# Kernel optimization log

Measured on AMD Instinct MI355X. Metric: run time of the kernel, lower is better.

## Reference

```python
import jax, jax.numpy as jnp
import numpy as np

N_NODES = 8192


def _gcn_norm(edge_index, num_nodes):
    # PyG GCNConv default: add self-loops, symmetric normalization.
    src, dst = edge_index[0], edge_index[1]
    loop = jnp.arange(num_nodes, dtype=src.dtype)
    src = jnp.concatenate([src, loop])
    dst = jnp.concatenate([dst, loop])
    deg = jax.ops.segment_sum(jnp.ones_like(dst, dtype=jnp.float32), dst,
                              num_segments=num_nodes)
    dis = jnp.where(deg > 0, jax.lax.rsqrt(jnp.maximum(deg, 1.0)), 0.0)
    norm = dis[src] * dis[dst]  # [E + N]
    return src, dst, norm


def _gcn_conv(x, W, b, src, dst, norm, num_nodes):
    h = x @ W                           # [N, F_out] dense GEMM
    msg = h[src] * norm[:, None]        # gather + scale, [E+N, F_out]
    out = jax.ops.segment_sum(msg, dst, num_segments=num_nodes)  # scatter-add
    return out + b


def setup_inputs() -> dict:
    key = jax.random.key(0)
    ks = jax.random.split(key, 8)
    N, E, F_in, H1, H2, F_out = N_NODES, 65536, 512, 4096, 1024, 10
    x = jax.random.normal(ks[0], (N, F_in), dtype=jnp.float32)
    edge_index = jax.random.randint(ks[1], (2, E), 0, N, dtype=jnp.int64)
    # Glorot-ish scaled weights
    W1 = jax.random.normal(ks[2], (F_in, H1), dtype=jnp.float32) * (1.0 / np.sqrt(F_in))
    b1 = jnp.zeros((H1,), dtype=jnp.float32)
    W2 = jax.random.normal(ks[3], (H1, H2), dtype=jnp.float32) * (1.0 / np.sqrt(H1))
    b2 = jnp.zeros((H2,), dtype=jnp.float32)
    W3 = jax.random.normal(ks[4], (H2, F_out), dtype=jnp.float32) * (1.0 / np.sqrt(H2))
    b3 = jnp.zeros((F_out,), dtype=jnp.float32)
    return {"x": x, "W1": W1, "b1": b1, "W2": W2, "b2": b2,
            "W3": W3, "b3": b3, "edge_index": edge_index}


def reference(x, W1, b1, W2, b2, W3, b3, edge_index):
    N = N_NODES
    src, dst, norm = _gcn_norm(edge_index, N)
    h = _gcn_conv(x.astype(jnp.float32), W1, b1, src, dst, norm, N)
    h = jax.nn.relu(h)  # dropout is identity in eval mode
    h = _gcn_conv(h, W2, b2, src, dst, norm, N)
    h = jax.nn.relu(h)
    h = _gcn_conv(h, W3, b3, src, dst, norm, N)
    return jax.nn.log_softmax(h, axis=1)
```

## Files before the change

### kernel.cpp

```cpp
#include <hip/hip_runtime.h>
#include <math.h>

#define N_NODES 8192
#define N_EDGES 65536
#define F_IN    512
#define HID1    4096
#define HID2    1024
#define F_OUT   10
#define H3_STRIDE 16
#define W3S_STRIDE 1032

typedef __bf16 bf16x8 __attribute__((ext_vector_type(8)));
typedef float floatx4 __attribute__((ext_vector_type(4)));

static __device__ __forceinline__ unsigned short f2bf(float f) {
    union { float f; unsigned u; } v; v.f = f;
    unsigned r = v.u + 0x7fffu + ((v.u >> 16) & 1u);
    return (unsigned short)(r >> 16);
}
static __device__ __forceinline__ float bf2f(unsigned short u) {
    union { unsigned u; float f; } v; v.u = ((unsigned)u) << 16;
    return v.f;
}

__global__ __launch_bounds__(1024) void hist_scan_kernel(
        const int* __restrict__ ei, int* __restrict__ deg,
        int* __restrict__ row_ptr, int* __restrict__ cnt) {
    __shared__ int hist[N_NODES];
    __shared__ int sums[1024];
    int t = threadIdx.x;
#pragma unroll
    for (int i = 0; i < 8; i++) hist[t + i * 1024] = 0;
    __syncthreads();
#pragma unroll
    for (int i = 0; i < 64; i++) {
        int d = ei[N_EDGES + i * 1024 + t];
        atomicAdd(&hist[d], 1);
    }
    __syncthreads();
    int base = t * 8;
    int local[8], run = 0;
#pragma unroll
    for (int i = 0; i < 8; i++) {
        int dv = hist[base + i];
        deg[base + i] = dv;
        cnt[base + i] = 0;
        local[i] = run; run += dv;
    }
    sums[t] = run;
    __syncthreads();
    for (int off = 1; off < 1024; off <<= 1) {
        int val = (t >= off) ? sums[t - off] : 0;
        __syncthreads();
        sums[t] += val;
        __syncthreads();
    }
    int offset = (t == 0) ? 0 : sums[t - 1];
#pragma unroll
    for (int i = 0; i < 8; i++) row_ptr[base + i] = offset + local[i];
    if (t == 1023) row_ptr[N_NODES] = sums[1023];
}

__global__ void fill_kernel(const int* __restrict__ ei, const int* __restrict__ deg,
                            const int* __restrict__ row_ptr, int* __restrict__ cnt,
                            int* __restrict__ csr_src, float* __restrict__ csr_w) {
    int e = blockIdx.x * blockDim.x + threadIdx.x;
    if (e < N_EDGES) {
        int s = ei[e];
        int d = ei[N_EDGES + e];
        int slot = row_ptr[d] + atomicAdd(&cnt[d], 1);
        csr_src[slot] = s;
        csr_w[slot] = rsqrtf((float)((deg[s] + 1) * (deg[d] + 1)));
    }
}

static __device__ __forceinline__ void transpose_body(
        const float* __restrict__ W, unsigned short* __restrict__ Wt,
        int K, int N, int k0, int n0, int tid, float (*t)[33]) {
    int c = tid & 31, r8 = tid >> 5;
#pragma unroll
    for (int i = 0; i < 4; i++) {
        int r = r8 + i * 8;
        t[r][c] = W[(size_t)(k0 + r) * N + n0 + c];
    }
    __syncthreads();
#pragma unroll
    for (int i = 0; i < 4; i++) {
        int r = r8 + i * 8;
        Wt[(size_t)(n0 + r) * K + k0 + c] = f2bf(t[c][r]);
    }
}

__global__ __launch_bounds__(256) void prep_kernel(
        const float* __restrict__ x, unsigned short* __restrict__ xb,
        const float* __restrict__ W1, unsigned short* __restrict__ W1t,
        const float* __restrict__ W2, unsigned short* __restrict__ W2t) {
    __shared__ float t[32][33];
    int b = blockIdx.x, tid = threadIdx.x;
    if (b < 4096) {
        int i = b * 256 + tid;
        float4 a = ((const float4*)x)[i];
        ushort4 o;
        o.x = f2bf(a.x); o.y = f2bf(a.y); o.z = f2bf(a.z); o.w = f2bf(a.w);
        ((ushort4*)xb)[i] = o;
    } else if (b < 6144) {
        int bb = b - 4096;
        transpose_body(W1, W1t, F_IN, HID1, (bb >> 7) * 32, (bb & 127) * 32, tid, t);
    } else {
        int bb = b - 6144;
        transpose_body(W2, W2t, HID1, HID2, (bb >> 5) * 32, (bb & 31) * 32, tid, t);
    }
}

__global__ __launch_bounds__(256) void agg1_kernel(
        const unsigned short* __restrict__ xb, const int* __restrict__ row_ptr,
        const int* __restrict__ csr_src, const float* __restrict__ csr_w,
        const int* __restrict__ deg, unsigned short* __restrict__ out) {
    int v = blockIdx.x * 2 + (threadIdx.x >> 7);
    int t = threadIdx.x & 127;
    const ushort4* x4 = (const ushort4*)xb;
    float sw = 1.0f / (float)(deg[v] + 1);
    ushort4 a = x4[(size_t)v * 128 + t];
    float ax = sw * bf2f(a.x), ay = sw * bf2f(a.y), az = sw * bf2f(a.z), aw = sw * bf2f(a.w);
    int e = row_ptr[v], end = row_ptr[v + 1];
    for (; e + 2 <= end; e += 2) {
        int s0 = csr_src[e], s1 = csr_src[e + 1];
        float w0 = csr_w[e], w1 = csr_w[e + 1];
        ushort4 b0 = x4[(size_t)s0 * 128 + t];
        ushort4 b1 = x4[(size_t)s1 * 128 + t];
        ax += w0 * bf2f(b0.x) + w1 * bf2f(b1.x);
        ay += w0 * bf2f(b0.y) + w1 * bf2f(b1.y);
        az += w0 * bf2f(b0.z) + w1 * bf2f(b1.z);
        aw += w0 * bf2f(b0.w) + w1 * bf2f(b1.w);
    }
    if (e < end) {
        int s = csr_src[e];
        float w = csr_w[e];
        ushort4 b = x4[(size_t)s * 128 + t];
        ax += w * bf2f(b.x); ay += w * bf2f(b.y); az += w * bf2f(b.z); aw += w * bf2f(b.w);
    }
    ushort4 o;
    o.x = f2bf(ax); o.y = f2bf(ay); o.z = f2bf(az); o.w = f2bf(aw);
    ((ushort4*)out)[(size_t)v * 128 + t] = o;
}

__global__ __launch_bounds__(256) void agg2_kernel(
        const unsigned short* __restrict__ h, const int* __restrict__ row_ptr,
        const int* __restrict__ csr_src, const float* __restrict__ csr_w,
        const int* __restrict__ deg, const float* __restrict__ bias,
        unsigned short* __restrict__ out) {
    int v = blockIdx.x;
    int t = threadIdx.x;
    const ushort4* h4 = (const ushort4*)h;
    float sw = 1.0f / (float)(deg[v] + 1);
    ushort4 a = h4[(size_t)v * 256 + t];
    float ax = sw * bf2f(a.x), ay = sw * bf2f(a.y), az = sw * bf2f(a.z), aw = sw * bf2f(a.w);
    int e = row_ptr[v], end = row_ptr[v + 1];
    for (; e + 2 <= end; e += 2) {
        int s0 = csr_src[e], s1 = csr_src[e + 1];
        float w0 = csr_w[e], w1 = csr_w[e + 1];
        ushort4 b0 = h4[(size_t)s0 * 256 + t];
        ushort4 b1 = h4[(size_t)s1 * 256 + t];
        ax += w0 * bf2f(b0.x) + w1 * bf2f(b1.x);
        ay += w0 * bf2f(b0.y) + w1 * bf2f(b1.y);
        az += w0 * bf2f(b0.z) + w1 * bf2f(b1.z);
        aw += w0 * bf2f(b0.w) + w1 * bf2f(b1.w);
    }
    if (e < end) {
        int s = csr_src[e];
        float w = csr_w[e];
        ushort4 b = h4[(size_t)s * 256 + t];
        ax += w * bf2f(b.x); ay += w * bf2f(b.y); az += w * bf2f(b.z); aw += w * bf2f(b.w);
    }
    float4 bb = ((const float4*)bias)[t];
    ushort4 o;
    o.x = f2bf(fmaxf(ax + bb.x, 0.0f)); o.y = f2bf(fmaxf(ay + bb.y, 0.0f));
    o.z = f2bf(fmaxf(az + bb.z, 0.0f)); o.w = f2bf(fmaxf(aw + bb.w, 0.0f));
    ((ushort4*)out)[(size_t)v * 256 + t] = o;
}

template <bool OUT_BF16, bool BIAS, bool RELU>
__global__ __launch_bounds__(256) void gemm_mfma_kernel(
        const unsigned short* __restrict__ A,
        const unsigned short* __restrict__ Bt,
        const float* __restrict__ bias,
        void* __restrict__ C,
        int M, int N, int K) {
    __shared__ unsigned short As[128 * 64];
    __shared__ unsigned short Bs[128 * 64];
    int tid = threadIdx.x;
    int wave = tid >> 6, lane = tid & 63;
    int wm = wave >> 1, wn = wave & 1;
    int GN = N >> 7;
    int b = blockIdx.x;
    int ntile = (b >> 3) % GN;
    int mtile = ((b >> 3) / GN) * 8 + (b & 7);
    int m0 = mtile * 128, n0 = ntile * 128;
    int lrow = lane & 15, lquad = lane >> 4;

    floatx4 acc[4][4] = {};

    for (int k0 = 0; k0 < K; k0 += 64) {
#pragma unroll
        for (int j = 0; j < 4; j++) {
            int idx = j * 256 + tid;
            int r = idx >> 3;
            int kc = (idx & 7) ^ (r & 7);
            __builtin_amdgcn_global_load_lds(
                (const __attribute__((address_space(1))) void*)(A + (size_t)(m0 + r) * K + k0 + kc * 8),
                (__attribute__((address_space(3))) void*)(&As[idx * 8]), 16, 0, 0);
            __builtin_amdgcn_global_load_lds(
                (const __attribute__((address_space(1))) void*)(Bt + (size_t)(n0 + r) * K + k0 + kc * 8),
                (__attribute__((address_space(3))) void*)(&Bs[idx * 8]), 16, 0, 0);
        }
        __syncthreads();
#pragma unroll
        for (int kk = 0; kk < 2; kk++) {
            bf16x8 af[4], bfr[4];
#pragma unroll
            for (int mt = 0; mt < 4; mt++) {
                int R = wm * 64 + mt * 16 + lrow;
                int c = kk * 4 + lquad;
                af[mt] = *(const bf16x8*)&As[(R * 8 + (c ^ (R & 7))) * 8];
            }
#pragma unroll
            for (int nt = 0; nt < 4; nt++) {
                int R = wn * 64 + nt * 16 + lrow;
                int c = kk * 4 + lquad;
                bfr[nt] = *(const bf16x8*)&Bs[(R * 8 + (c ^ (R & 7))) * 8];
            }
#pragma unroll
            for (int mt = 0; mt < 4; mt++)
#pragma unroll
                for (int nt = 0; nt < 4; nt++)
                    acc[mt][nt] = __builtin_amdgcn_mfma_f32_16x16x32_bf16(
                        af[mt], bfr[nt], acc[mt][nt], 0, 0, 0);
        }
        __syncthreads();
    }

#pragma unroll
    for (int mt = 0; mt < 4; mt++) {
#pragma unroll
        for (int nt = 0; nt < 4; nt++) {
            int col = n0 + wn * 64 + nt * 16 + lrow;
            float bv = BIAS ? bias[col] : 0.0f;
#pragma unroll
            for (int r = 0; r < 4; r++) {
                int row = m0 + wm * 64 + mt * 16 + lquad * 4 + r;
                float v = acc[mt][nt][r] + bv;
                if (RELU) v = fmaxf(v, 0.0f);
                if (OUT_BF16)
                    ((unsigned short*)C)[(size_t)row * N + col] = f2bf(v);
                else
                    ((float*)C)[(size_t)row * N + col] = v;
            }
        }
    }
}

__global__ __launch_bounds__(256) void gemm3_mfma_kernel(
        const unsigned short* __restrict__ A,
        const float* __restrict__ W3,
        float* __restrict__ H3) {
    __shared__ unsigned short w3s[16 * W3S_STRIDE];
    int tid = threadIdx.x;
    for (int i = tid; i < 16 * W3S_STRIDE; i += 256) w3s[i] = 0;
    __syncthreads();
    for (int i = tid; i < HID2 * F_OUT; i += 256) {
        int k = i / F_OUT, c = i % F_OUT;
        w3s[c * W3S_STRIDE + k] = f2bf(W3[i]);
    }
    __syncthreads();
    int wave = tid >> 6, lane = tid & 63;
    int lrow = lane & 15, lquad = lane >> 4;
    int m0 = (blockIdx.x * 4 + wave) * 16;
    floatx4 acc = {};
    const unsigned short* arow = A + (size_t)(m0 + lrow) * HID2 + lquad * 8;
#pragma unroll
    for (int kk = 0; kk < 32; kk++) {
        bf16x8 af = *(const bf16x8*)(arow + kk * 32);
        bf16x8 bf = *(const bf16x8*)&w3s[lrow * W3S_STRIDE + kk * 32 + lquad * 8];
        acc = __builtin_amdgcn_mfma_f32_16x16x32_bf16(af, bf, acc, 0, 0, 0);
    }
#pragma unroll
    for (int r = 0; r < 4; r++)
        H3[(size_t)(m0 + lquad * 4 + r) * H3_STRIDE + lrow] = acc[r];
}

__global__ void final_kernel(const float* __restrict__ h3, const int* __restrict__ row_ptr,
                             const int* __restrict__ csr_src, const float* __restrict__ csr_w,
                             const int* __restrict__ deg, const float* __restrict__ b3,
                             float* __restrict__ out) {
    int v = blockIdx.x * blockDim.x + threadIdx.x;
    if (v >= N_NODES) return;
    const float4* h4 = (const float4*)h3;
    float sw = 1.0f / (float)(deg[v] + 1);
    float a[12];
    *(float4*)&a[0] = h4[v * 4];
    *(float4*)&a[4] = h4[v * 4 + 1];
    *(float4*)&a[8] = h4[v * 4 + 2];
    float acc[F_OUT];
#pragma unroll
    for (int c = 0; c < F_OUT; c++) acc[c] = b3[c] + sw * a[c];
    int end = row_ptr[v + 1];
    for (int e = row_ptr[v]; e < end; e++) {
        int s = csr_src[e];
        float w = csr_w[e];
        float bsrc[12];
        *(float4*)&bsrc[0] = h4[s * 4];
        *(float4*)&bsrc[4] = h4[s * 4 + 1];
        *(float4*)&bsrc[8] = h4[s * 4 + 2];
#pragma unroll
        for (int c = 0; c < F_OUT; c++) acc[c] += w * bsrc[c];
    }
    float m = acc[0];
#pragma unroll
    for (int c = 1; c < F_OUT; c++) m = fmaxf(m, acc[c]);
    float ssum = 0.0f;
#pragma unroll
    for (int c = 0; c < F_OUT; c++) ssum += expf(acc[c] - m);
    float l = logf(ssum);
#pragma unroll
    for (int c = 0; c < F_OUT; c++) out[v * F_OUT + c] = acc[c] - m - l;
}

extern "C" void kernel_launch(void* const* d_in, const int* in_sizes, int n_in,
                              void* d_out, int out_size, void* d_ws, size_t ws_size,
                              hipStream_t stream) {
    const float* x  = (const float*)d_in[0];
    const float* W1 = (const float*)d_in[1];
    const float* b1 = (const float*)d_in[2];
    const float* W2 = (const float*)d_in[3];
    const float* b2 = (const float*)d_in[4];
    const float* W3 = (const float*)d_in[5];
    const float* b3 = (const float*)d_in[6];
    const int*   ei = (const int*)d_in[7];
    float* out = (float*)d_out;

    char* p = (char*)d_ws;
    int*   deg     = (int*)p;    p += N_NODES * 4;
    int*   cnt     = (int*)p;    p += N_NODES * 4;
    int*   row_ptr = (int*)p;    p += 33024;
    int*   csr_src = (int*)p;    p += N_EDGES * 4;
    float* csr_w   = (float*)p;  p += N_EDGES * 4;
    float* h3      = (float*)p;  p += N_NODES * H3_STRIDE * 4;
    unsigned short* xb    = (unsigned short*)p; p += (size_t)N_NODES * F_IN * 2;
    unsigned short* agg_x = (unsigned short*)p; p += (size_t)N_NODES * F_IN * 2;
    unsigned short* W1t   = (unsigned short*)p; p += (size_t)HID1 * F_IN * 2;
    unsigned short* W2t   = (unsigned short*)p; p += (size_t)HID2 * HID1 * 2;
    unsigned short* h1    = (unsigned short*)p; p += (size_t)N_NODES * HID1 * 2;
    unsigned short* h2pre = (unsigned short*)p; p += (size_t)N_NODES * HID2 * 2;
    unsigned short* agg2b = (unsigned short*)p; p += (size_t)N_NODES * HID2 * 2;

    hist_scan_kernel<<<1, 1024, 0, stream>>>(ei, deg, row_ptr, cnt);
    fill_kernel<<<N_EDGES / 256, 256, 0, stream>>>(ei, deg, row_ptr, cnt, csr_src, csr_w);

    prep_kernel<<<10240, 256, 0, stream>>>(x, xb, W1, W1t, W2, W2t);

    agg1_kernel<<<N_NODES / 2, 256, 0, stream>>>(xb, row_ptr, csr_src, csr_w, deg, agg_x);
    gemm_mfma_kernel<true, true, true><<<(HID1 / 128) * (N_NODES / 128), 256, 0, stream>>>(
        agg_x, W1t, b1, h1, N_NODES, HID1, F_IN);

    gemm_mfma_kernel<true, false, false><<<(HID2 / 128) * (N_NODES / 128), 256, 0, stream>>>(
        h1, W2t, nullptr, h2pre, N_NODES, HID2, HID1);
    agg2_kernel<<<N_NODES, 256, 0, stream>>>(h2pre, row_ptr, csr_src, csr_w, deg, b2, agg2b);

    gemm3_mfma_kernel<<<N_NODES / 64, 256, 0, stream>>>(agg2b, W3, h3);
    final_kernel<<<N_NODES / 256, 256, 0, stream>>>(h3, row_ptr, csr_src, csr_w, deg, b3, out);
}
```

Measured before the change: 302.0 us.

## Fuse agg2 with layer-3 GEMM, merge CSR fill into prep, widen gathers

```diff
diff --git a/kernel.cpp b/kernel.cpp
--- a/kernel.cpp
+++ b/kernel.cpp
@@ -8,7 +8,7 @@
 #define HID2    1024
 #define F_OUT   10
 #define H3_STRIDE 16
-#define W3S_STRIDE 1032
+#define W3B_STRIDE 1032
 
 typedef __bf16 bf16x8 __attribute__((ext_vector_type(8)));
 typedef float floatx4 __attribute__((ext_vector_type(4)));
@@ -21,6 +21,25 @@
 static __device__ __forceinline__ float bf2f(unsigned short u) {
     union { unsigned u; float f; } v; v.u = ((unsigned)u) << 16;
     return v.f;
+}
+static __device__ __forceinline__ void unpack8(uint4 r, float* f) {
+    union { unsigned u; float v; } c;
+    c.u = r.x << 16;          f[0] = c.v;
+    c.u = r.x & 0xffff0000u;  f[1] = c.v;
+    c.u = r.y << 16;          f[2] = c.v;
+    c.u = r.y & 0xffff0000u;  f[3] = c.v;
+    c.u = r.z << 16;          f[4] = c.v;
+    c.u = r.z & 0xffff0000u;  f[5] = c.v;
+    c.u = r.w << 16;          f[6] = c.v;
+    c.u = r.w & 0xffff0000u;  f[7] = c.v;
+}
+static __device__ __forceinline__ uint4 pack8(const float* f) {
+    uint4 o;
+    o.x = (unsigned)f2bf(f[0]) | ((unsigned)f2bf(f[1]) << 16);
+    o.y = (unsigned)f2bf(f[2]) | ((unsigned)f2bf(f[3]) << 16);
+    o.z = (unsigned)f2bf(f[4]) | ((unsigned)f2bf(f[5]) << 16);
+    o.w = (unsigned)f2bf(f[6]) | ((unsigned)f2bf(f[7]) << 16);
+    return o;
 }
 
 __global__ __launch_bounds__(1024) void hist_scan_kernel(
@@ -61,54 +80,57 @@
     if (t == 1023) row_ptr[N_NODES] = sums[1023];
 }
 
-__global__ void fill_kernel(const int* __restrict__ ei, const int* __restrict__ deg,
-                            const int* __restrict__ row_ptr, int* __restrict__ cnt,
-                            int* __restrict__ csr_src, float* __restrict__ csr_w) {
-    int e = blockIdx.x * blockDim.x + threadIdx.x;
-    if (e < N_EDGES) {
+static __device__ __forceinline__ void transpose_body(
+        const float* __restrict__ W, unsigned short* __restrict__ Wt,
+        int K, int N, int k0, int n0, int tid, float (*t)[33]) {
+    int c = tid & 31, r8 = tid >> 5;
+#pragma unroll
+    for (int i = 0; i < 4; i++) {
+        int r = r8 + i * 8;
+        t[r][c] = W[(size_t)(k0 + r) * N + n0 + c];
+    }
+    __syncthreads();
+#pragma unroll
+    for (int i = 0; i < 4; i++) {
+        int r = r8 + i * 8;
+        Wt[(size_t)(n0 + r) * K + k0 + c] = f2bf(t[c][r]);
+    }
+}
+
+__global__ __launch_bounds__(256) void megaprep_kernel(
+        const int* __restrict__ ei, const int* __restrict__ deg,
+        const int* __restrict__ row_ptr, int* __restrict__ cnt,
+        int* __restrict__ csr_src, float* __restrict__ csr_w,
+        const float* __restrict__ x, unsigned short* __restrict__ xb,
+        const float* __restrict__ W1, unsigned short* __restrict__ W1t,
+        const float* __restrict__ W2, unsigned short* __restrict__ W2t,
+        const float* __restrict__ W3, unsigned short* __restrict__ w3b) {
+    __shared__ float t[32][33];
+    int b = blockIdx.x, tid = threadIdx.x;
+    if (b < 256) {
+        int e = b * 256 + tid;
         int s = ei[e];
         int d = ei[N_EDGES + e];
         int slot = row_ptr[d] + atomicAdd(&cnt[d], 1);
         csr_src[slot] = s;
         csr_w[slot] = rsqrtf((float)((deg[s] + 1) * (deg[d] + 1)));
-    }
-}
-
-static __device__ __forceinline__ void transpose_body(
-        const float* __restrict__ W, unsigned short* __restrict__ Wt,
-        int K, int N, int k0, int n0, int tid, float (*t)[33]) {
-    int c = tid & 31, r8 = tid >> 5;
-#pragma unroll
-    for (int i = 0; i < 4; i++) {
-        int r = r8 + i * 8;
-        t[r][c] = W[(size_t)(k0 + r) * N + n0 + c];
-    }
-    __syncthreads();
-#pragma unroll
-    for (int i = 0; i < 4; i++) {
-        int r = r8 + i * 8;
-        Wt[(size_t)(n0 + r) * K + k0 + c] = f2bf(t[c][r]);
-    }
-}
-
-__global__ __launch_bounds__(256) void prep_kernel(
-        const float* __restrict__ x, unsigned short* __restrict__ xb,
-        const float* __restrict__ W1, unsigned short* __restrict__ W1t,
-        const float* __restrict__ W2, unsigned short* __restrict__ W2t) {
-    __shared__ float t[32][33];
-    int b = blockIdx.x, tid = threadIdx.x;
-    if (b < 4096) {
-        int i = b * 256 + tid;
+    } else if (b < 4352) {
+        int i = (b - 256) * 256 + tid;
         float4 a = ((const float4*)x)[i];
         ushort4 o;
         o.x = f2bf(a.x); o.y = f2bf(a.y); o.z = f2bf(a.z); o.w = f2bf(a.w);
         ((ushort4*)xb)[i] = o;
-    } else if (b < 6144) {
-        int bb = b - 4096;
+    } else if (b < 6400) {
+        int bb = b - 4352;
         transpose_body(W1, W1t, F_IN, HID1, (bb >> 7) * 32, (bb & 127) * 32, tid, t);
+    } else if (b < 10496) {
+        int bb = b - 6400;
+        transpose_body(W2, W2t, HID1, HID2, (bb >> 5) * 32, (bb & 31) * 32, tid, t);
     } else {
-        int bb = b - 6144;
-        transpose_body(W2, W2t, HID1, HID2, (bb >> 5) * 32, (bb & 31) * 32, tid, t);
+        for (int i = tid; i < HID2 * F_OUT; i += 256) {
+            int k = i / F_OUT, c = i % F_OUT;
+            w3b[c * W3B_STRIDE + k] = f2bf(W3[i]);
+        }
     }
 }
 
@@ -116,67 +138,105 @@
         const unsigned short* __restrict__ xb, const int* __restrict__ row_ptr,
         const int* __restrict__ csr_src, const float* __restrict__ csr_w,
         const int* __restrict__ deg, unsigned short* __restrict__ out) {
-    int v = blockIdx.x * 2 + (threadIdx.x >> 7);
-    int t = threadIdx.x & 127;
-    const ushort4* x4 = (const ushort4*)xb;
+    int v = blockIdx.x * 4 + (threadIdx.x >> 6);
+    int t = threadIdx.x & 63;
+    const uint4* xp = (const uint4*)xb;
     float sw = 1.0f / (float)(deg[v] + 1);
-    ushort4 a = x4[(size_t)v * 128 + t];
-    float ax = sw * bf2f(a.x), ay = sw * bf2f(a.y), az = sw * bf2f(a.z), aw = sw * bf2f(a.w);
+    float acc[8], tmp[8];
+    unpack8(xp[(size_t)v * 64 + t], tmp);
+#pragma unroll
+    for (int j = 0; j < 8; j++) acc[j] = sw * tmp[j];
     int e = row_ptr[v], end = row_ptr[v + 1];
     for (; e + 2 <= end; e += 2) {
         int s0 = csr_src[e], s1 = csr_src[e + 1];
         float w0 = csr_w[e], w1 = csr_w[e + 1];
-        ushort4 b0 = x4[(size_t)s0 * 128 + t];
-        ushort4 b1 = x4[(size_t)s1 * 128 + t];
-        ax += w0 * bf2f(b0.x) + w1 * bf2f(b1.x);
-        ay += w0 * bf2f(b0.y) + w1 * bf2f(b1.y);
-        az += w0 * bf2f(b0.z) + w1 * bf2f(b1.z);
-        aw += w0 * bf2f(b0.w) + w1 * bf2f(b1.w);
+        float f0[8], f1[8];
+        unpack8(xp[(size_t)s0 * 64 + t], f0);
+        unpack8(xp[(size_t)s1 * 64 + t], f1);
+#pragma unroll
+        for (int j = 0; j < 8; j++) acc[j] += w0 * f0[j] + w1 * f1[j];
     }
     if (e < end) {
         int s = csr_src[e];
         float w = csr_w[e];
-        ushort4 b = x4[(size_t)s * 128 + t];
-        ax += w * bf2f(b.x); ay += w * bf2f(b.y); az += w * bf2f(b.z); aw += w * bf2f(b.w);
-    }
-    ushort4 o;
-    o.x = f2bf(ax); o.y = f2bf(ay); o.z = f2bf(az); o.w = f2bf(aw);
-    ((ushort4*)out)[(size_t)v * 128 + t] = o;
-}
-
-__global__ __launch_bounds__(256) void agg2_kernel(
+        float f0[8];
+        unpack8(xp[(size_t)s * 64 + t], f0);
+#pragma unroll
+        for (int j = 0; j < 8; j++) acc[j] += w * f0[j];
+    }
+    ((uint4*)out)[(size_t)v * 64 + t] = pack8(acc);
+}
+
+__global__ __launch_bounds__(256) void agg2_gemm3_kernel(
         const unsigned short* __restrict__ h, const int* __restrict__ row_ptr,
         const int* __restrict__ csr_src, const float* __restrict__ csr_w,
-        const int* __restrict__ deg, const float* __restrict__ bias,
-        unsigned short* __restrict__ out) {
-    int v = blockIdx.x;
-    int t = threadIdx.x;
-    const ushort4* h4 = (const ushort4*)h;
+        const int* __restrict__ deg, const float* __restrict__ b2,
+        const unsigned short* __restrict__ w3b, float* __restrict__ H3) {
+    __shared__ unsigned short w3s[F_OUT * W3B_STRIDE];
+    __shared__ float red[4][F_OUT];
+    int tid = threadIdx.x;
+    for (int i = tid; i < F_OUT * W3B_STRIDE; i += 256) w3s[i] = w3b[i];
+    __syncthreads();
+    int half = tid >> 7;
+    int t = tid & 127;
+    int v = blockIdx.x * 2 + half;
+    const uint4* hp = (const uint4*)h;
     float sw = 1.0f / (float)(deg[v] + 1);
-    ushort4 a = h4[(size_t)v * 256 + t];
-    float ax = sw * bf2f(a.x), ay = sw * bf2f(a.y), az = sw * bf2f(a.z), aw = sw * bf2f(a.w);
+    float acc[8], tmp[8];
+    unpack8(hp[(size_t)v * 128 + t], tmp);
+#pragma unroll
+    for (int j = 0; j < 8; j++) acc[j] = sw * tmp[j];
     int e = row_ptr[v], end = row_ptr[v + 1];
     for (; e + 2 <= end; e += 2) {
         int s0 = csr_src[e], s1 = csr_src[e + 1];
         float w0 = csr_w[e], w1 = csr_w[e + 1];
-        ushort4 b0 = h4[(size_t)s0 * 256 + t];
-        ushort4 b1 = h4[(size_t)s1 * 256 + t];
-        ax += w0 * bf2f(b0.x) + w1 * bf2f(b1.x);
-        ay += w0 * bf2f(b0.y) + w1 * bf2f(b1.y);
-        az += w0 * bf2f(b0.z) + w1 * bf2f(b1.z);
-        aw += w0 * bf2f(b0.w) + w1 * bf2f(b1.w);
+        float f0[8], f1[8];
+        unpack8(hp[(size_t)s0 * 128 + t], f0);
+        unpack8(hp[(size_t)s1 * 128 + t], f1);
+#pragma unroll
+        for (int j = 0; j < 8; j++) acc[j] += w0 * f0[j] + w1 * f1[j];
     }
     if (e < end) {
         int s = csr_src[e];
         float w = csr_w[e];
-        ushort4 b = h4[(size_t)s * 256 + t];
-        ax += w * bf2f(b.x); ay += w * bf2f(b.y); az += w * bf2f(b.z); aw += w * bf2f(b.w);
-    }
-    float4 bb = ((const float4*)bias)[t];
-    ushort4 o;
-    o.x = f2bf(fmaxf(ax + bb.x, 0.0f)); o.y = f2bf(fmaxf(ay + bb.y, 0.0f));
-    o.z = f2bf(fmaxf(az + bb.z, 0.0f)); o.w = f2bf(fmaxf(aw + bb.w, 0.0f));
-    ((ushort4*)out)[(size_t)v * 256 + t] = o;
+        float f0[8];
+        unpack8(hp[(size_t)s * 128 + t], f0);
+#pragma unroll
+        for (int j = 0; j < 8; j++) acc[j] += w * f0[j];
+    }
+    float4 b4a = ((const float4*)b2)[t * 2];
+    float4 b4b = ((const float4*)b2)[t * 2 + 1];
+    acc[0] = fmaxf(acc[0] + b4a.x, 0.0f); acc[1] = fmaxf(acc[1] + b4a.y, 0.0f);
+    acc[2] = fmaxf(acc[2] + b4a.z, 0.0f); acc[3] = fmaxf(acc[3] + b4a.w, 0.0f);
+    acc[4] = fmaxf(acc[4] + b4b.x, 0.0f); acc[5] = fmaxf(acc[5] + b4b.y, 0.0f);
+    acc[6] = fmaxf(acc[6] + b4b.z, 0.0f); acc[7] = fmaxf(acc[7] + b4b.w, 0.0f);
+
+    float partial[F_OUT];
+#pragma unroll
+    for (int c = 0; c < F_OUT; c++) {
+        float wf[8];
+        unpack8(*(const uint4*)&w3s[c * W3B_STRIDE + t * 8], wf);
+        float pc = acc[0] * wf[0] + acc[1] * wf[1] + acc[2] * wf[2] + acc[3] * wf[3]
+                 + acc[4] * wf[4] + acc[5] * wf[5] + acc[6] * wf[6] + acc[7] * wf[7];
+        partial[c] = pc;
+    }
+#pragma unroll
+    for (int c = 0; c < F_OUT; c++) {
+#pragma unroll
+        for (int off = 32; off > 0; off >>= 1)
+            partial[c] += __shfl_xor(partial[c], off, 64);
+    }
+    int wave = tid >> 6, lane = tid & 63;
+    if (lane == 0) {
+#pragma unroll
+        for (int c = 0; c < F_OUT; c++) red[wave][c] = partial[c];
+    }
+    __syncthreads();
+    if (tid < 2 * F_OUT) {
+        int hh = tid / F_OUT, c = tid % F_OUT;
+        H3[(size_t)(blockIdx.x * 2 + hh) * H3_STRIDE + c] =
+            red[hh * 2][c] + red[hh * 2 + 1][c];
+    }
 }
 
 template <bool OUT_BF16, bool BIAS, bool RELU>
@@ -259,35 +319,6 @@
     }
 }
 
-__global__ __launch_bounds__(256) void gemm3_mfma_kernel(
-        const unsigned short* __restrict__ A,
-        const float* __restrict__ W3,
-        float* __restrict__ H3) {
-    __shared__ unsigned short w3s[16 * W3S_STRIDE];
-    int tid = threadIdx.x;
-    for (int i = tid; i < 16 * W3S_STRIDE; i += 256) w3s[i] = 0;
-    __syncthreads();
-    for (int i = tid; i < HID2 * F_OUT; i += 256) {
-        int k = i / F_OUT, c = i % F_OUT;
-        w3s[c * W3S_STRIDE + k] = f2bf(W3[i]);
-    }
-    __syncthreads();
-    int wave = tid >> 6, lane = tid & 63;
-    int lrow = lane & 15, lquad = lane >> 4;
-    int m0 = (blockIdx.x * 4 + wave) * 16;
-    floatx4 acc = {};
-    const unsigned short* arow = A + (size_t)(m0 + lrow) * HID2 + lquad * 8;
-#pragma unroll
-    for (int kk = 0; kk < 32; kk++) {
-        bf16x8 af = *(const bf16x8*)(arow + kk * 32);
-        bf16x8 bf = *(const bf16x8*)&w3s[lrow * W3S_STRIDE + kk * 32 + lquad * 8];
-        acc = __builtin_amdgcn_mfma_f32_16x16x32_bf16(af, bf, acc, 0, 0, 0);
-    }
-#pragma unroll
-    for (int r = 0; r < 4; r++)
-        H3[(size_t)(m0 + lquad * 4 + r) * H3_STRIDE + lrow] = acc[r];
-}
-
 __global__ void final_kernel(const float* __restrict__ h3, const int* __restrict__ row_ptr,
                              const int* __restrict__ csr_src, const float* __restrict__ csr_w,
                              const int* __restrict__ deg, const float* __restrict__ b3,
@@ -345,27 +376,27 @@
     int*   csr_src = (int*)p;    p += N_EDGES * 4;
     float* csr_w   = (float*)p;  p += N_EDGES * 4;
     float* h3      = (float*)p;  p += N_NODES * H3_STRIDE * 4;
+    unsigned short* w3b = (unsigned short*)p; p += (F_OUT * W3B_STRIDE * 2 + 255) / 256 * 256;
     unsigned short* xb    = (unsigned short*)p; p += (size_t)N_NODES * F_IN * 2;
     unsigned short* agg_x = (unsigned short*)p; p += (size_t)N_NODES * F_IN * 2;
     unsigned short* W1t   = (unsigned short*)p; p += (size_t)HID1 * F_IN * 2;
     unsigned short* W2t   = (unsigned short*)p; p += (size_t)HID2 * HID1 * 2;
     unsigned short* h1    = (unsigned short*)p; p += (size_t)N_NODES * HID1 * 2;
     unsigned short* h2pre = (unsigned short*)p; p += (size_t)N_NODES * HID2 * 2;
-    unsigned short* agg2b = (unsigned short*)p; p += (size_t)N_NODES * HID2 * 2;
 
     hist_scan_kernel<<<1, 1024, 0, stream>>>(ei, deg, row_ptr, cnt);
-    fill_kernel<<<N_EDGES / 256, 256, 0, stream>>>(ei, deg, row_ptr, cnt, csr_src, csr_w);
-
-    prep_kernel<<<10240, 256, 0, stream>>>(x, xb, W1, W1t, W2, W2t);
-
-    agg1_kernel<<<N_NODES / 2, 256, 0, stream>>>(xb, row_ptr, csr_src, csr_w, deg, agg_x);
+    megaprep_kernel<<<10497, 256, 0, stream>>>(ei, deg, row_ptr, cnt, csr_src, csr_w,
+                                               x, xb, W1, W1t, W2, W2t, W3, w3b);
+
+    agg1_kernel<<<N_NODES / 4, 256, 0, stream>>>(xb, row_ptr, csr_src, csr_w, deg, agg_x);
     gemm_mfma_kernel<true, true, true><<<(HID1 / 128) * (N_NODES / 128), 256, 0, stream>>>(
         agg_x, W1t, b1, h1, N_NODES, HID1, F_IN);
 
     gemm_mfma_kernel<true, false, false><<<(HID2 / 128) * (N_NODES / 128), 256, 0, stream>>>(
         h1, W2t, nullptr, h2pre, N_NODES, HID2, HID1);
-    agg2_kernel<<<N_NODES, 256, 0, stream>>>(h2pre, row_ptr, csr_src, csr_w, deg, b2, agg2b);
-
-    gemm3_mfma_kernel<<<N_NODES / 64, 256, 0, stream>>>(agg2b, W3, h3);
+
+    agg2_gemm3_kernel<<<N_NODES / 2, 256, 0, stream>>>(h2pre, row_ptr, csr_src, csr_w,
+                                                       deg, b2, w3b, h3);
+
     final_kernel<<<N_NODES / 256, 256, 0, stream>>>(h3, row_ptr, csr_src, csr_w, deg, b3, out);
 }
```

Measured after the change: 304.0 us. About the same (+0.7%).
